# Kernel tuning notes

Hardware: AMD Instinct MI355X
Metric: run time of the kernel (lower is better)

Reference implementation:

```python
import jax, jax.numpy as jnp
import numpy as np

NUM_BINS = 64
Z_MIN, Z_MAX = -3.0, 1.0
BIN_SIZE = (Z_MAX - Z_MIN) / NUM_BINS
EPS_MEAN = 1e-5
EPS_BN = 1e-5


def setup_inputs() -> dict:
    key = jax.random.key(0)
    k1, k2, k3, k4 = jax.random.split(key, 4)
    M, N, C = 100000, 64, 4
    feat_channels, out_dim = 64, NUM_BINS * 3
    features = jax.random.normal(k1, (M, N, C), dtype=jnp.float32)
    num_points = jax.random.randint(k2, (M,), 0, 65, dtype=jnp.int32)
    coors = jax.random.randint(k3, (M, 4), 0, 100, dtype=jnp.int32)
    W = jax.random.normal(k4, (feat_channels, out_dim), dtype=jnp.float32) * (1.0 / np.sqrt(out_dim))
    b = jnp.zeros((feat_channels,), dtype=jnp.float32)
    gamma = jnp.ones((feat_channels,), dtype=jnp.float32)
    beta = jnp.zeros((feat_channels,), dtype=jnp.float32)
    return {"features": features, "num_points": num_points, "coors": coors,
            "W": W, "b": b, "gamma": gamma, "beta": beta}


def reference(features, num_points, coors, W, b, gamma, beta):
    M, N, C = features.shape
    # validity mask per point
    mask = (jnp.arange(N)[None, :] < num_points[:, None]).astype(features.dtype)  # [M, N]
    z = features[..., 2]  # [M, N]
    r = features[..., 3]  # [M, N]
    bin_idx = jnp.clip(((z - Z_MIN) / BIN_SIZE).astype(jnp.int32), 0, NUM_BINS - 1)  # [M, N]

    rows = jnp.arange(M)[:, None]  # [M, 1] broadcast against [M, N]
    zeros = jnp.zeros((M, NUM_BINS), dtype=features.dtype)
    count = zeros.at[rows, bin_idx].add(mask)
    sum_z = zeros.at[rows, bin_idx].add(z * mask)
    sum_r = zeros.at[rows, bin_idx].add(r * mask)
    mean_z = sum_z / (count + EPS_MEAN)
    mean_r = sum_r / (count + EPS_MEAN)

    # interleaved layout [count, mean_z, mean_r] per bin -> [M, 3*NUM_BINS]
    hist = jnp.stack([count, mean_z, mean_r], axis=-1).reshape(M, NUM_BINS * 3)

    # Linear -> BatchNorm1d (training: biased batch stats) -> ReLU
    x = hist @ W.T + b  # [M, feat_channels]
    mu = jnp.mean(x, axis=0)
    var = jnp.mean((x - mu) ** 2, axis=0)
    xn = (x - mu) / jnp.sqrt(var + EPS_BN)
    return jax.nn.relu(xn * gamma + beta)
```

## Files before the change

### kernel.cpp

```cpp
#include <hip/hip_runtime.h>
#include <hip/hip_bf16.h>
#include <math.h>


typedef __attribute__((ext_vector_type(8))) short bf16x8;
typedef __attribute__((ext_vector_type(4))) float f32x4;
typedef __attribute__((ext_vector_type(4))) int   i32x4;

#define ZMINF   (-3.0f)
#define INV_BIN 16.0f
#define QS      8192.0f
#define INV_QS  (1.0f / 8192.0f)
#define PBIASF  65536.0f
#define PBIASI  65536
#define CBIT    16777216
#define TSC     16777216.0f
#define INV_TSC (1.0f / 16777216.0f)
#define REPS    16
#define RSTRIDE 66

__device__ __forceinline__ short f2bf(float f) {
    __hip_bfloat16 h = __float2bfloat16(f);
    return __builtin_bit_cast(short, h);
}

__global__ __launch_bounds__(256)
void k0_prep(const float* __restrict__ W,
             short*       __restrict__ wsW,
             unsigned long long* __restrict__ totals)
{
    const int tid    = blockIdx.x * 256 + threadIdx.x;
    const int stride = gridDim.x * 256;
    for (int e = tid; e < 24 * 64 * 8; e += stride) {
        const int j  = e & 7;
        const int ln = (e >> 3) & 63;
        const int st = e >> 9;
        const int s  = st >> 2, t = st & 3;
        const int k  = s * 32 + (ln >> 4) * 8 + j;
        const int n  = t * 16 + (ln & 15);
        const int wc = (k < 64) ? 3 * k
                     : (k < 128) ? 3 * (k - 64) + 1
                                 : 3 * (k - 128) + 2;
        wsW[e] = f2bf(W[n * 192 + wc]);
    }
    for (int e = tid; e < REPS * 128; e += stride) totals[e] = 0ull;
}

__global__ __launch_bounds__(128, 8)
void k1_hist_mfma(const uint2*  __restrict__ feat2,
                  const int*    __restrict__ nump,
                  const bf16x8* __restrict__ wsWf,
                  const float*  __restrict__ bvec,
                  float*        __restrict__ xout,
                  unsigned long long* __restrict__ totals,
                  int M)
{
    __shared__ unsigned long long sH[16 * RSTRIDE];

    const int tid  = threadIdx.x;
    const int wave = tid >> 6;
    const int lane = tid & 63;
    const int col  = lane & 15;
    const int quad = lane >> 4;
    const int half = wave;

    const int gbase = blockIdx.x * 16;
    float psum[2] = {0.f, 0.f};
    float psq[2]  = {0.f, 0.f};
    bf16x8 bcur[2];

    if (gbase < M) {
        uint2 zw[8];
        const int npv = nump[min(gbase + half * 8 + (lane & 7), M - 1)];
        #pragma unroll
        for (int uu = 0; uu < 8; ++uu) {
            const int rc = min(gbase + half * 8 + uu, M - 1);
            zw[uu] = feat2[((size_t)rc * 64 + lane) * 2 + 1];
        }

        {
            i32x4* p4 = (i32x4*)&sH[(size_t)half * 8 * RSTRIDE];
            #pragma unroll
            for (int i = 0; i < 5; ++i) {
                const int idx = lane + i * 64;
                if (idx < (8 * RSTRIDE * 2) / 4) p4[idx] = i32x4{0, 0, 0, 0};
            }
        }
        __builtin_amdgcn_wave_barrier();

        #pragma unroll
        for (int uu = 0; uu < 8; ++uu) {
            const int u = half * 8 + uu;
            int np_u = __builtin_amdgcn_readlane(npv, uu);
            np_u = (gbase + u < M) ? np_u : 0;
            if (lane < np_u) {
                const float z  = __int_as_float((int)zw[uu].x);
                const float rr = __int_as_float((int)zw[uu].y);
                int bi = (int)((z - ZMINF) * INV_BIN);
                bi = min(max(bi, 0), 63);
                const unsigned long long add =
                    ((unsigned long long)(unsigned)(CBIT + PBIASI + (int)(z * QS)) << 32)
                    | (unsigned)(PBIASI + (int)(rr * QS));
                atomicAdd(&sH[u * RSTRIDE + bi], add);
            }
        }

        bcur[0] = wsWf[(half * 2 + 0) * 64 + lane];
        bcur[1] = wsWf[(half * 2 + 1) * 64 + lane];
    }

    __syncthreads();

    if (gbase < M) {
        f32x4 acc[2] = {};
        bf16x8 bnxt[2];
        const int* ar = (const int*)sH + col * (RSTRIDE * 2);
        #pragma unroll
        for (int g = 0; g < 2; ++g) {
            const int o0 = g * 32 + quad * 8;
            const i32x4* ap = (const i32x4*)(ar + 2 * o0);
            const i32x4 a0 = ap[0], a1 = ap[1], a2 = ap[2], a3 = ap[3];
            const int zz[8]  = {a0.y, a0.w, a1.y, a1.w, a2.y, a2.w, a3.y, a3.w};
            const int rrw[8] = {a0.x, a0.z, a1.x, a1.z, a2.x, a2.z, a3.x, a3.z};
            float cnt[8], rcp[8], av[8];
            bf16x8 af;

            bnxt[0] = wsWf[((2 + g) * 4 + half * 2 + 0) * 64 + lane];
            bnxt[1] = wsWf[((2 + g) * 4 + half * 2 + 1) * 64 + lane];
            #pragma unroll
            for (int j = 0; j < 8; ++j) { cnt[j] = (float)(zz[j] >> 24); av[j] = cnt[j]; }
            #pragma unroll
            for (int j = 0; j < 8; ++j) af[j] = f2bf(av[j]);
            acc[0] = __builtin_amdgcn_mfma_f32_16x16x32_bf16(af, bcur[0], acc[0], 0, 0, 0);
            acc[1] = __builtin_amdgcn_mfma_f32_16x16x32_bf16(af, bcur[1], acc[1], 0, 0, 0);
            bcur[0] = bnxt[0]; bcur[1] = bnxt[1];

            bnxt[0] = wsWf[((4 + g) * 4 + half * 2 + 0) * 64 + lane];
            bnxt[1] = wsWf[((4 + g) * 4 + half * 2 + 1) * 64 + lane];
            #pragma unroll
            for (int j = 0; j < 8; ++j) {
                rcp[j] = __builtin_amdgcn_rcpf(cnt[j] + 1e-5f) * INV_QS;
                const float pay = (float)(zz[j] & 0xFFFFFF);
                av[j] = (pay - cnt[j] * PBIASF) * rcp[j];
            }
            #pragma unroll
            for (int j = 0; j < 8; ++j) af[j] = f2bf(av[j]);
            acc[0] = __builtin_amdgcn_mfma_f32_16x16x32_bf16(af, bcur[0], acc[0], 0, 0, 0);
            acc[1] = __builtin_amdgcn_mfma_f32_16x16x32_bf16(af, bcur[1], acc[1], 0, 0, 0);
            bcur[0] = bnxt[0]; bcur[1] = bnxt[1];

            if (g == 0) {
                bnxt[0] = wsWf[(1 * 4 + half * 2 + 0) * 64 + lane];
                bnxt[1] = wsWf[(1 * 4 + half * 2 + 1) * 64 + lane];
            }
            #pragma unroll
            for (int j = 0; j < 8; ++j)
                av[j] = ((float)rrw[j] - cnt[j] * PBIASF) * rcp[j];
            #pragma unroll
            for (int j = 0; j < 8; ++j) af[j] = f2bf(av[j]);
            acc[0] = __builtin_amdgcn_mfma_f32_16x16x32_bf16(af, bcur[0], acc[0], 0, 0, 0);
            acc[1] = __builtin_amdgcn_mfma_f32_16x16x32_bf16(af, bcur[1], acc[1], 0, 0, 0);
            bcur[0] = bnxt[0]; bcur[1] = bnxt[1];
        }

        #pragma unroll
        for (int tt = 0; tt < 2; ++tt) {
            const int t = half * 2 + tt;
            const float bias = bvec[t * 16 + col];
            #pragma unroll
            for (int i = 0; i < 4; ++i) {
                const int row = gbase + quad * 4 + i;
                if (row < M) {
                    const float xv = acc[tt][i] + bias;
                    xout[(size_t)row * 64 + t * 16 + col] = xv;
                    psum[tt] += xv;
                    psq[tt]  += xv * xv;
                }
            }
        }
    }

    #pragma unroll
    for (int tt = 0; tt < 2; ++tt) {
        psum[tt] += __shfl_xor(psum[tt], 16);
        psum[tt] += __shfl_xor(psum[tt], 32);
        psq[tt]  += __shfl_xor(psq[tt], 16);
        psq[tt]  += __shfl_xor(psq[tt], 32);
    }
    const float myS = (quad & 1) ? psum[1] : psum[0];
    const float myQ = (quad & 1) ? psq[1]  : psq[0];
    const int gw = blockIdx.x * 2 + wave;
    if (lane < 32) {
        unsigned long long* dst = totals + (gw & (REPS - 1)) * 128 + half * 32 + lane;
        atomicAdd(dst,      (unsigned long long)(long long)(myS * TSC));
        atomicAdd(dst + 64, (unsigned long long)(long long)(myQ * TSC));
    }
}

__global__ __launch_bounds__(256)
void k3_bn_apply(float4* __restrict__ x,
                 const unsigned long long* __restrict__ totals,
                 const float* __restrict__ gamma,
                 const float* __restrict__ beta,
                 float invM, int n4)
{
    __shared__ float sT[128];
    __shared__ float sa[64];
    __shared__ float sc[64];
    const int t = threadIdx.x;
    if (t < 128) {
        long long s = 0;
        #pragma unroll
        for (int rep = 0; rep < REPS; ++rep) s += (long long)totals[rep * 128 + t];
        sT[t] = (float)s * (invM * INV_TSC);
    }
    __syncthreads();
    if (t < 64) {
        const float mu   = sT[t];
        const float q    = sT[64 + t];
        const float var  = q - mu * mu;
        const float rstd = 1.0f / sqrtf(var + 1e-5f);
        const float a    = gamma[t] * rstd;
        sa[t] = a;
        sc[t] = beta[t] - mu * a;
    }
    __syncthreads();
    const int stride = gridDim.x * 256;
    for (int i = blockIdx.x * 256 + t; i < n4; i += stride) {
        const float4 a = ((const float4*)sa)[i & 15];
        const float4 c = ((const float4*)sc)[i & 15];
        float4 v = x[i];
        v.x = fmaxf(fmaf(v.x, a.x, c.x), 0.f);
        v.y = fmaxf(fmaf(v.y, a.y, c.y), 0.f);
        v.z = fmaxf(fmaf(v.z, a.z, c.z), 0.f);
        v.w = fmaxf(fmaf(v.w, a.w, c.w), 0.f);
        x[i] = v;
    }
}

extern "C" void kernel_launch(void* const* d_in, const int* in_sizes, int n_in,
                              void* d_out, int out_size, void* d_ws, size_t ws_size,
                              hipStream_t stream) {
    const uint2*  feat2 = (const uint2*)d_in[0];
    const int*    nump  = (const int*)d_in[1];
    const float*  W     = (const float*)d_in[3];
    const float*  bvec  = (const float*)d_in[4];
    const float*  gamma = (const float*)d_in[5];
    const float*  beta  = (const float*)d_in[6];

    const int M = in_sizes[1];
    float* xout = (float*)d_out;
    short* wsW  = (short*)d_ws;
    unsigned long long* totals =
        (unsigned long long*)((char*)d_ws + 24 * 64 * 8 * sizeof(short));

    k0_prep<<<16, 256, 0, stream>>>(W, wsW, totals);

    const int nblk = (M + 15) / 16;
    k1_hist_mfma<<<nblk, 128, 0, stream>>>(feat2, nump, (const bf16x8*)wsW, bvec, xout, totals, M);

    const int n4 = out_size / 4;
    const int nblk3 = (n4 + 256 * 16 - 1) / (256 * 16);
    k3_bn_apply<<<nblk3, 256, 0, stream>>>((float4*)d_out, totals, gamma, beta,
                                           1.0f / (float)M, n4);
}
```

Before: 185.0 us.

## Fuse BN apply into histogram-MFMA kernel via grid-wide barrier

Merges the histogram/MFMA linear kernel with the BatchNorm-apply kernel. Each block now processes 4 tiles of 16 rows and keeps the pre-BN activations in registers. Blocks publish their partial sums, then spin on a global atomic counter until every block has arrived, and write the normalized ReLU output directly. This removes the intermediate write and re-read of the full activation matrix plus one kernel launch. In exchange, every block must be co-resident on the GPU or the spin barrier deadlocks, and all output stores are delayed until after the barrier.

New measurement: 404.4 us. 2.19x slower.

```diff
diff --git a/kernel.cpp b/kernel.cpp
--- a/kernel.cpp
+++ b/kernel.cpp
@@ -18,6 +18,7 @@
 #define INV_TSC (1.0f / 16777216.0f)
 #define REPS    16
 #define RSTRIDE 66
+#define TILES   4
 
 __device__ __forceinline__ short f2bf(float f) {
     __hip_bfloat16 h = __float2bfloat16(f);
@@ -43,140 +44,148 @@
                                  : 3 * (k - 128) + 2;
         wsW[e] = f2bf(W[n * 192 + wc]);
     }
-    for (int e = tid; e < REPS * 128; e += stride) totals[e] = 0ull;
-}
-
-__global__ __launch_bounds__(128, 8)
-void k1_hist_mfma(const uint2*  __restrict__ feat2,
-                  const int*    __restrict__ nump,
-                  const bf16x8* __restrict__ wsWf,
-                  const float*  __restrict__ bvec,
-                  float*        __restrict__ xout,
-                  unsigned long long* __restrict__ totals,
-                  int M)
+    for (int e = tid; e < REPS * 128 + 1; e += stride) totals[e] = 0ull;
+}
+
+__global__ __launch_bounds__(128, 4)
+void k1_fused(const uint2*  __restrict__ feat2,
+              const int*    __restrict__ nump,
+              const bf16x8* __restrict__ wsWf,
+              const float*  __restrict__ bvec,
+              const float*  __restrict__ gamma,
+              const float*  __restrict__ beta,
+              float*        __restrict__ out,
+              unsigned long long* __restrict__ totals,
+              unsigned int* __restrict__ ctr,
+              float invM, int M)
 {
     __shared__ unsigned long long sH[16 * RSTRIDE];
 
     const int tid  = threadIdx.x;
-    const int wave = tid >> 6;
+    const int half = tid >> 6;
     const int lane = tid & 63;
     const int col  = lane & 15;
     const int quad = lane >> 4;
-    const int half = wave;
-
-    const int gbase = blockIdx.x * 16;
+
+    const int gbase0 = blockIdx.x * (16 * TILES);
+
+    const float bias0 = bvec[(half * 2 + 0) * 16 + col];
+    const float bias1 = bvec[(half * 2 + 1) * 16 + col];
+
     float psum[2] = {0.f, 0.f};
     float psq[2]  = {0.f, 0.f};
-    bf16x8 bcur[2];
-
-    if (gbase < M) {
-        uint2 zw[8];
-        const int npv = nump[min(gbase + half * 8 + (lane & 7), M - 1)];
-        #pragma unroll
-        for (int uu = 0; uu < 8; ++uu) {
-            const int rc = min(gbase + half * 8 + uu, M - 1);
-            zw[uu] = feat2[((size_t)rc * 64 + lane) * 2 + 1];
-        }
-
-        {
-            i32x4* p4 = (i32x4*)&sH[(size_t)half * 8 * RSTRIDE];
-            #pragma unroll
-            for (int i = 0; i < 5; ++i) {
-                const int idx = lane + i * 64;
-                if (idx < (8 * RSTRIDE * 2) / 4) p4[idx] = i32x4{0, 0, 0, 0};
-            }
-        }
-        __builtin_amdgcn_wave_barrier();
-
-        #pragma unroll
-        for (int uu = 0; uu < 8; ++uu) {
-            const int u = half * 8 + uu;
-            int np_u = __builtin_amdgcn_readlane(npv, uu);
-            np_u = (gbase + u < M) ? np_u : 0;
-            if (lane < np_u) {
-                const float z  = __int_as_float((int)zw[uu].x);
-                const float rr = __int_as_float((int)zw[uu].y);
-                int bi = (int)((z - ZMINF) * INV_BIN);
-                bi = min(max(bi, 0), 63);
-                const unsigned long long add =
-                    ((unsigned long long)(unsigned)(CBIT + PBIASI + (int)(z * QS)) << 32)
-                    | (unsigned)(PBIASI + (int)(rr * QS));
-                atomicAdd(&sH[u * RSTRIDE + bi], add);
-            }
-        }
-
-        bcur[0] = wsWf[(half * 2 + 0) * 64 + lane];
-        bcur[1] = wsWf[(half * 2 + 1) * 64 + lane];
-    }
-
-    __syncthreads();
-
-    if (gbase < M) {
-        f32x4 acc[2] = {};
-        bf16x8 bnxt[2];
-        const int* ar = (const int*)sH + col * (RSTRIDE * 2);
-        #pragma unroll
-        for (int g = 0; g < 2; ++g) {
-            const int o0 = g * 32 + quad * 8;
-            const i32x4* ap = (const i32x4*)(ar + 2 * o0);
-            const i32x4 a0 = ap[0], a1 = ap[1], a2 = ap[2], a3 = ap[3];
-            const int zz[8]  = {a0.y, a0.w, a1.y, a1.w, a2.y, a2.w, a3.y, a3.w};
-            const int rrw[8] = {a0.x, a0.z, a1.x, a1.z, a2.x, a2.z, a3.x, a3.z};
-            float cnt[8], rcp[8], av[8];
-            bf16x8 af;
-
-            bnxt[0] = wsWf[((2 + g) * 4 + half * 2 + 0) * 64 + lane];
-            bnxt[1] = wsWf[((2 + g) * 4 + half * 2 + 1) * 64 + lane];
-            #pragma unroll
-            for (int j = 0; j < 8; ++j) { cnt[j] = (float)(zz[j] >> 24); av[j] = cnt[j]; }
-            #pragma unroll
-            for (int j = 0; j < 8; ++j) af[j] = f2bf(av[j]);
-            acc[0] = __builtin_amdgcn_mfma_f32_16x16x32_bf16(af, bcur[0], acc[0], 0, 0, 0);
-            acc[1] = __builtin_amdgcn_mfma_f32_16x16x32_bf16(af, bcur[1], acc[1], 0, 0, 0);
-            bcur[0] = bnxt[0]; bcur[1] = bnxt[1];
-
-            bnxt[0] = wsWf[((4 + g) * 4 + half * 2 + 0) * 64 + lane];
-            bnxt[1] = wsWf[((4 + g) * 4 + half * 2 + 1) * 64 + lane];
-            #pragma unroll
-            for (int j = 0; j < 8; ++j) {
-                rcp[j] = __builtin_amdgcn_rcpf(cnt[j] + 1e-5f) * INV_QS;
-                const float pay = (float)(zz[j] & 0xFFFFFF);
-                av[j] = (pay - cnt[j] * PBIASF) * rcp[j];
-            }
-            #pragma unroll
-            for (int j = 0; j < 8; ++j) af[j] = f2bf(av[j]);
-            acc[0] = __builtin_amdgcn_mfma_f32_16x16x32_bf16(af, bcur[0], acc[0], 0, 0, 0);
-            acc[1] = __builtin_amdgcn_mfma_f32_16x16x32_bf16(af, bcur[1], acc[1], 0, 0, 0);
-            bcur[0] = bnxt[0]; bcur[1] = bnxt[1];
-
-            if (g == 0) {
-                bnxt[0] = wsWf[(1 * 4 + half * 2 + 0) * 64 + lane];
-                bnxt[1] = wsWf[(1 * 4 + half * 2 + 1) * 64 + lane];
-            }
-            #pragma unroll
-            for (int j = 0; j < 8; ++j)
-                av[j] = ((float)rrw[j] - cnt[j] * PBIASF) * rcp[j];
-            #pragma unroll
-            for (int j = 0; j < 8; ++j) af[j] = f2bf(av[j]);
-            acc[0] = __builtin_amdgcn_mfma_f32_16x16x32_bf16(af, bcur[0], acc[0], 0, 0, 0);
-            acc[1] = __builtin_amdgcn_mfma_f32_16x16x32_bf16(af, bcur[1], acc[1], 0, 0, 0);
-            bcur[0] = bnxt[0]; bcur[1] = bnxt[1];
-        }
-
-        #pragma unroll
-        for (int tt = 0; tt < 2; ++tt) {
-            const int t = half * 2 + tt;
-            const float bias = bvec[t * 16 + col];
+    f32x4 acc[TILES][2];
+
+    #pragma unroll
+    for (int t = 0; t < TILES; ++t) {
+        const int gbase = gbase0 + t * 16;
+        if (gbase < M) {
+            uint2 zw[8];
+            const int npv = nump[min(gbase + half * 8 + (lane & 7), M - 1)];
+            #pragma unroll
+            for (int uu = 0; uu < 8; ++uu) {
+                const int rc = min(gbase + half * 8 + uu, M - 1);
+                zw[uu] = feat2[((size_t)rc * 64 + lane) * 2 + 1];
+            }
+
+            {
+                i32x4* p4 = (i32x4*)&sH[(size_t)half * 8 * RSTRIDE];
+                #pragma unroll
+                for (int i = 0; i < 5; ++i) {
+                    const int idx = lane + i * 64;
+                    if (idx < (8 * RSTRIDE * 2) / 4) p4[idx] = i32x4{0, 0, 0, 0};
+                }
+            }
+            __builtin_amdgcn_wave_barrier();
+
+            #pragma unroll
+            for (int uu = 0; uu < 8; ++uu) {
+                const int u = half * 8 + uu;
+                int np_u = __builtin_amdgcn_readlane(npv, uu);
+                np_u = (gbase + u < M) ? np_u : 0;
+                if (lane < np_u) {
+                    const float z  = __int_as_float((int)zw[uu].x);
+                    const float rr = __int_as_float((int)zw[uu].y);
+                    int bi = (int)((z - ZMINF) * INV_BIN);
+                    bi = min(max(bi, 0), 63);
+                    const unsigned long long add =
+                        ((unsigned long long)(unsigned)(CBIT + PBIASI + (int)(z * QS)) << 32)
+                        | (unsigned)(PBIASI + (int)(rr * QS));
+                    atomicAdd(&sH[u * RSTRIDE + bi], add);
+                }
+            }
+
+            bf16x8 bcur[2], bnxt[2];
+            bcur[0] = wsWf[(half * 2 + 0) * 64 + lane];
+            bcur[1] = wsWf[(half * 2 + 1) * 64 + lane];
+
+            __syncthreads();
+
+            f32x4 a0v = {}, a1v = {};
+            const int* ar = (const int*)sH + col * (RSTRIDE * 2);
+            #pragma unroll
+            for (int g = 0; g < 2; ++g) {
+                const int o0 = g * 32 + quad * 8;
+                const i32x4* ap = (const i32x4*)(ar + 2 * o0);
+                const i32x4 b0 = ap[0], b1 = ap[1], b2 = ap[2], b3 = ap[3];
+                const int zz[8]  = {b0.y, b0.w, b1.y, b1.w, b2.y, b2.w, b3.y, b3.w};
+                const int rrw[8] = {b0.x, b0.z, b1.x, b1.z, b2.x, b2.z, b3.x, b3.z};
+                float cnt[8], rcp[8], av[8];
+                bf16x8 af;
+
+                bnxt[0] = wsWf[((2 + g) * 4 + half * 2 + 0) * 64 + lane];
+                bnxt[1] = wsWf[((2 + g) * 4 + half * 2 + 1) * 64 + lane];
+                #pragma unroll
+                for (int j = 0; j < 8; ++j) { cnt[j] = (float)(zz[j] >> 24); av[j] = cnt[j]; }
+                #pragma unroll
+                for (int j = 0; j < 8; ++j) af[j] = f2bf(av[j]);
+                a0v = __builtin_amdgcn_mfma_f32_16x16x32_bf16(af, bcur[0], a0v, 0, 0, 0);
+                a1v = __builtin_amdgcn_mfma_f32_16x16x32_bf16(af, bcur[1], a1v, 0, 0, 0);
+                bcur[0] = bnxt[0]; bcur[1] = bnxt[1];
+
+                bnxt[0] = wsWf[((4 + g) * 4 + half * 2 + 0) * 64 + lane];
+                bnxt[1] = wsWf[((4 + g) * 4 + half * 2 + 1) * 64 + lane];
+                #pragma unroll
+                for (int j = 0; j < 8; ++j) {
+                    rcp[j] = __builtin_amdgcn_rcpf(cnt[j] + 1e-5f) * INV_QS;
+                    const float pay = (float)(zz[j] & 0xFFFFFF);
+                    av[j] = (pay - cnt[j] * PBIASF) * rcp[j];
+                }
+                #pragma unroll
+                for (int j = 0; j < 8; ++j) af[j] = f2bf(av[j]);
+                a0v = __builtin_amdgcn_mfma_f32_16x16x32_bf16(af, bcur[0], a0v, 0, 0, 0);
+                a1v = __builtin_amdgcn_mfma_f32_16x16x32_bf16(af, bcur[1], a1v, 0, 0, 0);
+                bcur[0] = bnxt[0]; bcur[1] = bnxt[1];
+
+                if (g == 0) {
+                    bnxt[0] = wsWf[(1 * 4 + half * 2 + 0) * 64 + lane];
+                    bnxt[1] = wsWf[(1 * 4 + half * 2 + 1) * 64 + lane];
+                }
+                #pragma unroll
+                for (int j = 0; j < 8; ++j)
+                    av[j] = ((float)rrw[j] - cnt[j] * PBIASF) * rcp[j];
+                #pragma unroll
+                for (int j = 0; j < 8; ++j) af[j] = f2bf(av[j]);
+                a0v = __builtin_amdgcn_mfma_f32_16x16x32_bf16(af, bcur[0], a0v, 0, 0, 0);
+                a1v = __builtin_amdgcn_mfma_f32_16x16x32_bf16(af, bcur[1], a1v, 0, 0, 0);
+                bcur[0] = bnxt[0]; bcur[1] = bnxt[1];
+            }
+
             #pragma unroll
             for (int i = 0; i < 4; ++i) {
                 const int row = gbase + quad * 4 + i;
+                const float xv0 = a0v[i] + bias0;
+                const float xv1 = a1v[i] + bias1;
+                acc[t][0][i] = xv0;
+                acc[t][1][i] = xv1;
                 if (row < M) {
-                    const float xv = acc[tt][i] + bias;
-                    xout[(size_t)row * 64 + t * 16 + col] = xv;
-                    psum[tt] += xv;
-                    psq[tt]  += xv * xv;
-                }
-            }
+                    psum[0] += xv0; psq[0] += xv0 * xv0;
+                    psum[1] += xv1; psq[1] += xv1 * xv1;
+                }
+            }
+
+            if (t + 1 < TILES)
+                __syncthreads();
         }
     }
 
@@ -189,52 +198,53 @@
     }
     const float myS = (quad & 1) ? psum[1] : psum[0];
     const float myQ = (quad & 1) ? psq[1]  : psq[0];
-    const int gw = blockIdx.x * 2 + wave;
     if (lane < 32) {
-        unsigned long long* dst = totals + (gw & (REPS - 1)) * 128 + half * 32 + lane;
+        unsigned long long* dst = totals + (blockIdx.x & (REPS - 1)) * 128 + half * 32 + lane;
         atomicAdd(dst,      (unsigned long long)(long long)(myS * TSC));
         atomicAdd(dst + 64, (unsigned long long)(long long)(myQ * TSC));
     }
-}
-
-__global__ __launch_bounds__(256)
-void k3_bn_apply(float4* __restrict__ x,
-                 const unsigned long long* __restrict__ totals,
-                 const float* __restrict__ gamma,
-                 const float* __restrict__ beta,
-                 float invM, int n4)
-{
-    __shared__ float sT[128];
-    __shared__ float sa[64];
-    __shared__ float sc[64];
-    const int t = threadIdx.x;
-    if (t < 128) {
-        long long s = 0;
+
+    __syncthreads();
+    if (tid == 0) {
+        __hip_atomic_fetch_add(ctr, 1u, __ATOMIC_ACQ_REL, __HIP_MEMORY_SCOPE_AGENT);
+        while (__hip_atomic_load(ctr, __ATOMIC_ACQUIRE, __HIP_MEMORY_SCOPE_AGENT)
+               < (unsigned)gridDim.x)
+            __builtin_amdgcn_s_sleep(8);
+    }
+    __syncthreads();
+
+    float aco[2], cco[2];
+    #pragma unroll
+    for (int tt = 0; tt < 2; ++tt) {
+        const int ch = (half * 2 + tt) * 16 + col;
+        long long S = 0, Q = 0;
         #pragma unroll
-        for (int rep = 0; rep < REPS; ++rep) s += (long long)totals[rep * 128 + t];
-        sT[t] = (float)s * (invM * INV_TSC);
-    }
-    __syncthreads();
-    if (t < 64) {
-        const float mu   = sT[t];
-        const float q    = sT[64 + t];
+        for (int rep = 0; rep < REPS; ++rep) {
+            S += (long long)totals[rep * 128 + ch];
+            Q += (long long)totals[rep * 128 + 64 + ch];
+        }
+        const float mu   = (float)S * (invM * INV_TSC);
+        const float q    = (float)Q * (invM * INV_TSC);
         const float var  = q - mu * mu;
         const float rstd = 1.0f / sqrtf(var + 1e-5f);
-        const float a    = gamma[t] * rstd;
-        sa[t] = a;
-        sc[t] = beta[t] - mu * a;
-    }
-    __syncthreads();
-    const int stride = gridDim.x * 256;
-    for (int i = blockIdx.x * 256 + t; i < n4; i += stride) {
-        const float4 a = ((const float4*)sa)[i & 15];
-        const float4 c = ((const float4*)sc)[i & 15];
-        float4 v = x[i];
-        v.x = fmaxf(fmaf(v.x, a.x, c.x), 0.f);
-        v.y = fmaxf(fmaf(v.y, a.y, c.y), 0.f);
-        v.z = fmaxf(fmaf(v.z, a.z, c.z), 0.f);
-        v.w = fmaxf(fmaf(v.w, a.w, c.w), 0.f);
-        x[i] = v;
+        const float a    = gamma[ch] * rstd;
+        aco[tt] = a;
+        cco[tt] = beta[ch] - mu * a;
+    }
+    #pragma unroll
+    for (int t = 0; t < TILES; ++t) {
+        const int gbase = gbase0 + t * 16;
+        if (gbase < M) {
+            #pragma unroll
+            for (int i = 0; i < 4; ++i) {
+                const int row = gbase + quad * 4 + i;
+                if (row < M) {
+                    float* xr = out + (size_t)row * 64 + half * 32 + col;
+                    xr[0]  = fmaxf(fmaf(acc[t][0][i], aco[0], cco[0]), 0.f);
+                    xr[16] = fmaxf(fmaf(acc[t][1][i], aco[1], cco[1]), 0.f);
+                }
+            }
+        }
     }
 }
 
@@ -249,18 +259,14 @@
     const float*  beta  = (const float*)d_in[6];
 
     const int M = in_sizes[1];
-    float* xout = (float*)d_out;
     short* wsW  = (short*)d_ws;
     unsigned long long* totals =
         (unsigned long long*)((char*)d_ws + 24 * 64 * 8 * sizeof(short));
+    unsigned int* ctr = (unsigned int*)(totals + REPS * 128);
 
     k0_prep<<<16, 256, 0, stream>>>(W, wsW, totals);
 
-    const int nblk = (M + 15) / 16;
-    k1_hist_mfma<<<nblk, 128, 0, stream>>>(feat2, nump, (const bf16x8*)wsW, bvec, xout, totals, M);
-
-    const int n4 = out_size / 4;
-    const int nblk3 = (n4 + 256 * 16 - 1) / (256 * 16);
-    k3_bn_apply<<<nblk3, 256, 0, stream>>>((float4*)d_out, totals, gamma, beta,
-                                           1.0f / (float)M, n4);
-}
+    const int nblk = (M + 16 * TILES - 1) / (16 * TILES);
+    k1_fused<<<nblk, 128, 0, stream>>>(feat2, nump, (const bf16x8*)wsW, bvec, gamma, beta,
+                                       (float*)d_out, totals, ctr, 1.0f / (float)M, M);
+}
```
